# Kernel tuning notes

Measured on AMD Instinct MI355X. Metric: run time of the kernel, lower is better.

Reference implementation:

```python
import jax, jax.numpy as jnp
import numpy as np

B, L, D, C = 1, 512, 128, 128  # batch, length, input_dim, channel_dim


def _layernorm(x, w, b, eps=1e-5):
    mu = jnp.mean(x, axis=-1, keepdims=True)
    var = jnp.var(x, axis=-1, keepdims=True)
    return (x - mu) * jax.lax.rsqrt(var + eps) * w + b


def setup_inputs() -> dict:
    key = jax.random.key(0)
    ks = jax.random.split(key, 12)
    s = 0.05  # weight scale ~ xavier for d=128
    f32 = jnp.float32
    return {
        "z": jax.random.normal(ks[0], (B, L, L, D), f32),
        "ln_in_w": jnp.ones((D,), f32), "ln_in_b": jnp.zeros((D,), f32),
        "Wga": jax.random.normal(ks[1], (D, C), f32) * s, "bga": jnp.zeros((C,), f32),
        "Wla": jax.random.normal(ks[2], (D, C), f32) * s, "bla": jnp.zeros((C,), f32),
        "Wgb": jax.random.normal(ks[3], (D, C), f32) * s, "bgb": jnp.zeros((C,), f32),
        "Wlb": jax.random.normal(ks[4], (D, C), f32) * s, "blb": jnp.zeros((C,), f32),
        "ln_o_w": jnp.ones((C,), f32), "ln_o_b": jnp.zeros((C,), f32),
        "Wgo": jax.random.normal(ks[5], (D, D), f32) * s, "bgo": jnp.zeros((D,), f32),
        "Wlo": jax.random.normal(ks[6], (C, D), f32) * s, "blo": jnp.zeros((D,), f32),
    }


def reference(z, ln_in_w, ln_in_b, Wga, bga, Wla, bla, Wgb, bgb, Wlb, blb,
              ln_o_w, ln_o_b, Wgo, bgo, Wlo, blo):
    # z: [B, L, L, D]
    zn = _layernorm(z, ln_in_w, ln_in_b)
    a = jax.nn.sigmoid(zn @ Wga + bga) * (zn @ Wla + bla)   # [B,L,L,C]
    b = jax.nn.sigmoid(zn @ Wgb + bgb) * (zn @ Wlb + blb)   # [B,L,L,C]
    # triangular update (axis=1): per-channel L x L matmul
    # k[b,i,j,c] = sum_m a[b,i,m,c] * b[b,m,j,c]
    k = jnp.einsum('bimc,bmjc->bijc', a, b)
    out = jax.nn.sigmoid(zn @ Wgo + bgo) * (_layernorm(k, ln_o_w, ln_o_b) @ Wlo + blo)
    return out
```

## Files before the change

### kernel.cpp

```cpp
#include <hip/hip_runtime.h>

typedef unsigned short u16;
typedef __attribute__((ext_vector_type(8))) short bf16x8;
typedef __attribute__((ext_vector_type(4))) float f32x4;

#define L_ 512
#define D_ 128
#define LL_ (512*512)
#define LP_ 136
#define TP_ 72

#define WT_OFF 0
#define B2_OFF 98304
#define ZN_OFF (B2_OFF + 1536)
#define AT2_OFF (ZN_OFF + 128*LL_)
#define BT2_OFF (AT2_OFF + 128*LL_)
#define KT2_OFF (BT2_OFF + 128*LL_)
#define WS2_NEED_BYTES ((size_t)(KT2_OFF + 128*LL_) * 2)
#define AT1_OFF (B2_OFF + 1536)
#define BT1_OFF (AT1_OFF + 128*LL_)
#define KT1_OFF (BT1_OFF + 128*LL_)

union U16x8 { uint4 u4; bf16x8 v; u16 s[8]; };
union U16x4 { ushort4 v; u16 s[4]; };

__device__ __forceinline__ u16 f2bf(float f){
  union { float f; unsigned int i; } w; w.f = f;
  unsigned int r = w.i + 0x7FFFu + ((w.i >> 16) & 1u);
  return (u16)(r >> 16);
}
__device__ __forceinline__ float sigm(float x){
  return 1.0f / (1.0f + __expf(-x));
}

__global__ __launch_bounds__(256) void conv_kernel(
    const float* __restrict__ Wga, const float* __restrict__ Wla,
    const float* __restrict__ Wgb, const float* __restrict__ Wlb,
    const float* __restrict__ Wgo, const float* __restrict__ Wlo,
    const float* __restrict__ lnw, const float* __restrict__ lnb,
    const float* __restrict__ onw, const float* __restrict__ onb,
    const float* __restrict__ bga, const float* __restrict__ bla,
    const float* __restrict__ bgb, const float* __restrict__ blb,
    const float* __restrict__ bgo, const float* __restrict__ blo,
    u16* __restrict__ wt, float* __restrict__ bias2)
{
  if (blockIdx.x < 384){
    int idx = blockIdx.x*256 + threadIdx.x;
    int w = idx >> 14, rem = idx & 16383, n = rem >> 7, k = rem & 127;
    const float* src;
    switch (w){
      case 0: src = Wga; break; case 1: src = Wla; break; case 2: src = Wgb; break;
      case 3: src = Wlb; break; case 4: src = Wgo; break; default: src = Wlo;
    }
    float sc = (w == 5) ? onw[k] : lnw[k];
    wt[idx] = f2bf(src[k*128 + n] * sc);
  } else {
    int j = (blockIdx.x - 384)*256 + threadIdx.x;
    int w = j >> 7, n = j & 127;
    const float* src; const float* bs;
    switch (w){
      case 0: src = Wga; bs = bga; break; case 1: src = Wla; bs = bla; break;
      case 2: src = Wgb; bs = bgb; break; case 3: src = Wlb; bs = blb; break;
      case 4: src = Wgo; bs = bgo; break; default: src = Wlo; bs = blo;
    }
    const float* lb = (w == 5) ? onb : lnb;
    float acc = bs[n];
    for (int k = 0; k < 128; ++k) acc += lb[k] * src[k*128 + n];
    bias2[j] = acc;
  }
}

__global__ __launch_bounds__(256) void stageZ_kernel(
    const float* __restrict__ z, u16* __restrict__ zn_g)
{
  const int t = threadIdx.x, r = t >> 1, h = t & 1;
  const int row = blockIdx.x*128 + r;
  const float* zrow = z + (long)row*D_ + h*64;
  float raw[64];
  float sum = 0.f, sq = 0.f;
#pragma unroll
  for (int q = 0; q < 16; ++q){
    float4 v = *(const float4*)(zrow + q*4);
    raw[q*4+0] = v.x; raw[q*4+1] = v.y; raw[q*4+2] = v.z; raw[q*4+3] = v.w;
    sum += v.x + v.y + v.z + v.w;
    sq  += v.x*v.x + v.y*v.y + v.z*v.z + v.w*v.w;
  }
  sum += __shfl_xor(sum, 1, 64);
  sq  += __shfl_xor(sq , 1, 64);
  float mu = sum * (1.f/128.f);
  float rstd = rsqrtf(sq*(1.f/128.f) - mu*mu + 1e-5f);
  u16* orow = zn_g + (long)row*D_ + h*64;
#pragma unroll
  for (int q = 0; q < 8; ++q){
    U16x8 o;
#pragma unroll
    for (int e = 0; e < 8; ++e)
      o.s[e] = f2bf(raw[q*8+e] - mu > 0 ? (raw[q*8+e] - mu)*rstd : (raw[q*8+e] - mu)*rstd);
    *(uint4*)(orow + q*8) = o.u4;
  }
}

__device__ __forceinline__ void gemm128(const u16* znlds, const u16* __restrict__ wtm,
                                        int wm, int wn, int quad, int l16, f32x4 acc[4][4])
{
  bf16x8 bf[4][4];
#pragma unroll
  for (int nt = 0; nt < 4; ++nt){
    int n = wn*64 + nt*16 + l16;
#pragma unroll
    for (int kc = 0; kc < 4; ++kc){
      U16x8 u; u.u4 = *(const uint4*)(wtm + n*128 + kc*32 + quad*8);
      bf[nt][kc] = u.v;
    }
  }
#pragma unroll
  for (int mt = 0; mt < 4; ++mt){
    int row = wm*64 + mt*16 + l16;
    bf16x8 af[4];
#pragma unroll
    for (int kc = 0; kc < 4; ++kc)
      af[kc] = *(const bf16x8*)(znlds + row*LP_ + kc*32 + quad*8);
#pragma unroll
    for (int nt = 0; nt < 4; ++nt)
#pragma unroll
      for (int kc = 0; kc < 4; ++kc)
        acc[mt][nt] = __builtin_amdgcn_mfma_f32_16x16x32_bf16(af[kc], bf[nt][kc], acc[mt][nt], 0, 0, 0);
  }
}

__device__ __forceinline__ void gemm128s(const u16* znS, const u16* __restrict__ wtm,
                                         int wm, int wn, int quad, int l16, f32x4 acc[4][4])
{
  bf16x8 bf[4][4];
#pragma unroll
  for (int nt = 0; nt < 4; ++nt){
    int n = wn*64 + nt*16 + l16;
#pragma unroll
    for (int kc = 0; kc < 4; ++kc){
      U16x8 u; u.u4 = *(const uint4*)(wtm + n*128 + kc*32 + quad*8);
      bf[nt][kc] = u.v;
    }
  }
  const int r7 = l16 & 7;
#pragma unroll
  for (int mt = 0; mt < 4; ++mt){
    int row = wm*64 + mt*16 + l16;
    bf16x8 af[4];
#pragma unroll
    for (int kc = 0; kc < 4; ++kc)
      af[kc] = *(const bf16x8*)(znS + row*128 + (((kc*4 + quad) ^ r7) << 3));
#pragma unroll
    for (int nt = 0; nt < 4; ++nt)
#pragma unroll
      for (int kc = 0; kc < 4; ++kc)
        acc[mt][nt] = __builtin_amdgcn_mfma_f32_16x16x32_bf16(af[kc], bf[nt][kc], acc[mt][nt], 0, 0, 0);
  }
}

__device__ __forceinline__ void gemm64(const u16* alds, const u16* __restrict__ wtm,
                                       int wm, int wn, int quad, int l16, f32x4 acc[2][4])
{
  bf16x8 bf[4][4];
#pragma unroll
  for (int nt = 0; nt < 4; ++nt){
    int n = wn*64 + nt*16 + l16;
#pragma unroll
    for (int kc = 0; kc < 4; ++kc){
      U16x8 u; u.u4 = *(const uint4*)(wtm + n*128 + kc*32 + quad*8);
      bf[nt][kc] = u.v;
    }
  }
#pragma unroll
  for (int mt = 0; mt < 2; ++mt){
    int row = wm*32 + mt*16 + l16;
    bf16x8 af[4];
#pragma unroll
    for (int kc = 0; kc < 4; ++kc)
      af[kc] = *(const bf16x8*)(alds + row*LP_ + kc*32 + quad*8);
#pragma unroll
    for (int nt = 0; nt < 4; ++nt)
#pragma unroll
      for (int kc = 0; kc < 4; ++kc)
        acc[mt][nt] = __builtin_amdgcn_mfma_f32_16x16x32_bf16(af[kc], bf[nt][kc], acc[mt][nt], 0, 0, 0);
  }
}

__global__ __launch_bounds__(256) void stageA2_kernel(
    const u16* __restrict__ zn_g, const u16* __restrict__ wt,
    const float* __restrict__ bias2,
    u16* __restrict__ a_t, u16* __restrict__ b_tt)
{
  __shared__ __align__(16) u16 znS[128*128];

  const int bid = blockIdx.x;
  const int type = bid >> 11;
  const int tile = bid & 2047;
  const int outer = tile >> 2;
  const int seg = tile & 3;

  const int t = threadIdx.x;
  const int r = t >> 1, h = t & 1;
  const int lane = t & 63, wave = t >> 6;
  const int quad = lane >> 4, l16 = lane & 15;
  const int wm = wave & 1, wn = wave >> 1;

  {
    const int lr = lane >> 4, lc = lane & 15;
    const int r7s = (wave*4 + lr) & 7;
    const int cgx = lc ^ r7s;
#pragma unroll
    for (int q = 0; q < 8; ++q){
      int row = q*16 + wave*4 + lr;
      int gpos = (type == 0) ? (outer*L_ + seg*128 + row) : ((seg*128 + row)*L_ + outer);
      __builtin_amdgcn_global_load_lds(
          (const __attribute__((address_space(1))) void*)(zn_g + (long)gpos*D_ + cgx*8),
          (__attribute__((address_space(3))) void*)(&znS[(q*16 + wave*4)*128]),
          16, 0, 0);
    }
  }
  __syncthreads();

  const u16* wg   = wt + (type ? 2 : 0)*16384;
  const u16* wl   = wt + (type ? 3 : 1)*16384;
  const float* bgp = bias2 + (type ? 2 : 0)*128;
  const float* blp = bias2 + (type ? 3 : 1)*128;
  const f32x4 z4 = {0.f, 0.f, 0.f, 0.f};

  f32x4 accG[4][4], accL[4][4];
#pragma unroll
  for (int mt = 0; mt < 4; ++mt)
#pragma unroll
    for (int nt = 0; nt < 4; ++nt){ accG[mt][nt] = z4; accL[mt][nt] = z4; }

  gemm128s(znS, wg, wm, wn, quad, l16, accG);
#pragma unroll
  for (int nt = 0; nt < 4; ++nt){
    float bb = bgp[wn*64 + nt*16 + l16];
#pragma unroll
    for (int mt = 0; mt < 4; ++mt)
#pragma unroll
      for (int e = 0; e < 4; ++e)
        accG[mt][nt][e] = sigm(accG[mt][nt][e] + bb);
  }
  gemm128s(znS, wl, wm, wn, quad, l16, accL);
#pragma unroll
  for (int nt = 0; nt < 4; ++nt){
    float bb = blp[wn*64 + nt*16 + l16];
#pragma unroll
    for (int mt = 0; mt < 4; ++mt)
#pragma unroll
      for (int e = 0; e < 4; ++e)
        accG[mt][nt][e] *= (accL[mt][nt][e] + bb);
  }

  __syncthreads();

  u16* trh = znS;
  u16* dst = type ? b_tt : a_t;
  const int base = outer*L_ + seg*128;
#pragma unroll
  for (int pass = 0; pass < 2; ++pass){
    if (wm == pass){
#pragma unroll
      for (int nt = 0; nt < 4; ++nt){
        int gcol = wn*64 + nt*16 + l16;
#pragma unroll
        for (int mt = 0; mt < 4; ++mt){
          U16x4 pk;
#pragma unroll
          for (int e = 0; e < 4; ++e)
            pk.s[e] = f2bf(accG[mt][nt][e]);
          *(ushort4*)(trh + gcol*TP_ + mt*16 + quad*4) = pk.v;
        }
      }
    }
    __syncthreads();
#pragma unroll
    for (int q = 0; q < 4; ++q){
      uint4 v = *(const uint4*)(trh + r*TP_ + h*32 + q*8);
      *(uint4*)(dst + r*LL_ + base + pass*64 + h*32 + q*8) = v;
    }
    __syncthreads();
  }
}

__global__ __launch_bounds__(256) void stageA_kernel(
    const float* __restrict__ z, const u16* __restrict__ wt,
    const float* __restrict__ bias2,
    u16* __restrict__ a_t, u16* __restrict__ b_tt)
{
  __shared__ __align__(16) u16 smem[128*LP_];
  u16* zn = smem;
  u16* trh = smem;

  const int bid = blockIdx.x;
  const int type = bid >> 11;
  const int tile = bid & 2047;
  const int outer = tile >> 2;
  const int seg = tile & 3;

  const int t = threadIdx.x;
  const int r = t >> 1, h = t & 1;
  const int lane = t & 63, wave = t >> 6;
  const int quad = lane >> 4, l16 = lane & 15;
  const int wm = wave & 1, wn = wave >> 1;

  {
    int gpos = (type == 0) ? (outer*L_ + seg*128 + r) : ((seg*128 + r)*L_ + outer);
    const float* zrow = z + gpos*D_ + h*64;
    float raw[64];
    float sum = 0.f, sq = 0.f;
#pragma unroll
    for (int q = 0; q < 16; ++q){
      float4 v = *(const float4*)(zrow + q*4);
      raw[q*4+0] = v.x; raw[q*4+1] = v.y; raw[q*4+2] = v.z; raw[q*4+3] = v.w;
      sum += v.x + v.y + v.z + v.w;
      sq  += v.x*v.x + v.y*v.y + v.z*v.z + v.w*v.w;
    }
    sum += __shfl_xor(sum, 1, 64);
    sq  += __shfl_xor(sq , 1, 64);
    float mu = sum * (1.f/128.f);
    float rstd = rsqrtf(sq*(1.f/128.f) - mu*mu + 1e-5f);
#pragma unroll
    for (int q = 0; q < 8; ++q){
      U16x8 o;
#pragma unroll
      for (int e = 0; e < 8; ++e)
        o.s[e] = f2bf((raw[q*8+e] - mu)*rstd);
      *(uint4*)(zn + r*LP_ + h*64 + q*8) = o.u4;
    }
  }
  __syncthreads();

  const u16* wg   = wt + (type ? 2 : 0)*16384;
  const u16* wl   = wt + (type ? 3 : 1)*16384;
  const float* bgp = bias2 + (type ? 2 : 0)*128;
  const float* blp = bias2 + (type ? 3 : 1)*128;
  const f32x4 z4 = {0.f, 0.f, 0.f, 0.f};

  f32x4 accG[4][4], accL[4][4];
#pragma unroll
  for (int mt = 0; mt < 4; ++mt)
#pragma unroll
    for (int nt = 0; nt < 4; ++nt){ accG[mt][nt] = z4; accL[mt][nt] = z4; }

  gemm128(zn, wg, wm, wn, quad, l16, accG);
#pragma unroll
  for (int nt = 0; nt < 4; ++nt){
    float bb = bgp[wn*64 + nt*16 + l16];
#pragma unroll
    for (int mt = 0; mt < 4; ++mt)
#pragma unroll
      for (int e = 0; e < 4; ++e)
        accG[mt][nt][e] = sigm(accG[mt][nt][e] + bb);
  }
  gemm128(zn, wl, wm, wn, quad, l16, accL);
#pragma unroll
  for (int nt = 0; nt < 4; ++nt){
    float bb = blp[wn*64 + nt*16 + l16];
#pragma unroll
    for (int mt = 0; mt < 4; ++mt)
#pragma unroll
      for (int e = 0; e < 4; ++e)
        accG[mt][nt][e] *= (accL[mt][nt][e] + bb);
  }

  __syncthreads();

  u16* dst = type ? b_tt : a_t;
  const int base = outer*L_ + seg*128;
#pragma unroll
  for (int pass = 0; pass < 2; ++pass){
    if (wm == pass){
#pragma unroll
      for (int nt = 0; nt < 4; ++nt){
        int gcol = wn*64 + nt*16 + l16;
#pragma unroll
        for (int mt = 0; mt < 4; ++mt){
          U16x4 pk;
#pragma unroll
          for (int e = 0; e < 4; ++e)
            pk.s[e] = f2bf(accG[mt][nt][e]);
          *(ushort4*)(trh + gcol*TP_ + mt*16 + quad*4) = pk.v;
        }
      }
    }
    __syncthreads();
#pragma unroll
    for (int q = 0; q < 4; ++q){
      uint4 v = *(const uint4*)(trh + r*TP_ + h*32 + q*8);
      *(uint4*)(dst + r*LL_ + base + pass*64 + h*32 + q*8) = v;
    }
    __syncthreads();
  }
}

__global__ __launch_bounds__(256) void stageT_kernel(
    const u16* __restrict__ a_t, const u16* __restrict__ b_tt, u16* __restrict__ k_t)
{
  __shared__ __align__(16) u16 As[128*64];
  __shared__ __align__(16) u16 Bs[128*64];
  const int bid = blockIdx.x;
  const int lid = (bid & 7)*256 + (bid >> 3);
  const int c = lid >> 4, it = (lid >> 2) & 3, jt = lid & 3;
  const u16* Ab = a_t + c*LL_ + it*128*L_;
  const u16* Bb = b_tt + c*LL_ + jt*128*L_;
  const int t = threadIdx.x;
  const int lane = t & 63, wave = t >> 6;
  const int quad = lane >> 4, l16 = lane & 15;
  const int wm = wave & 1, wn = wave >> 1;
  const int sr8 = lane >> 3, scl = lane & 7;
  const int cgx = scl ^ sr8;
  const int swz = (l16 & 7) << 3;

  f32x4 acc[4][4];
  const f32x4 z4 = {0.f,0.f,0.f,0.f};
#pragma unroll
  for (int mt = 0; mt < 4; ++mt)
#pragma unroll
    for (int nt = 0; nt < 4; ++nt) acc[mt][nt] = z4;

  for (int kt = 0; kt < 8; ++kt){
    const int k0 = kt*64;
#pragma unroll
    for (int q = 0; q < 4; ++q){
      int row = q*32 + wave*8 + sr8;
      __builtin_amdgcn_global_load_lds(
          (const __attribute__((address_space(1))) void*)(Ab + row*L_ + k0 + cgx*8),
          (__attribute__((address_space(3))) void*)(&As[(q*32 + wave*8)*64]),
          16, 0, 0);
    }
#pragma unroll
    for (int q = 0; q < 4; ++q){
      int row = q*32 + wave*8 + sr8;
      __builtin_amdgcn_global_load_lds(
          (const __attribute__((address_space(1))) void*)(Bb + row*L_ + k0 + cgx*8),
          (__attribute__((address_space(3))) void*)(&Bs[(q*32 + wave*8)*64]),
          16, 0, 0);
    }
    __syncthreads();
    bf16x8 bfr[4][2];
#pragma unroll
    for (int nt = 0; nt < 4; ++nt){
      int brow = wn*64 + nt*16 + l16;
#pragma unroll
      for (int ks = 0; ks < 2; ++ks)
        bfr[nt][ks] = *(const bf16x8*)(Bs + brow*64 + (((ks*4 + quad)*8) ^ swz));
    }
#pragma unroll
    for (int mt = 0; mt < 4; ++mt){
      int arow = wm*64 + mt*16 + l16;
      bf16x8 af[2];
#pragma unroll
      for (int ks = 0; ks < 2; ++ks)
        af[ks] = *(const bf16x8*)(As + arow*64 + (((ks*4 + quad)*8) ^ swz));
#pragma unroll
      for (int nt = 0; nt < 4; ++nt)
#pragma unroll
        for (int ks = 0; ks < 2; ++ks)
          acc[mt][nt] = __builtin_amdgcn_mfma_f32_16x16x32_bf16(af[ks], bfr[nt][ks], acc[mt][nt], 0, 0, 0);
    }
    __syncthreads();
  }

#pragma unroll
  for (int mt = 0; mt < 4; ++mt)
#pragma unroll
    for (int nt = 0; nt < 4; ++nt){
      int gcol = wn*64 + nt*16 + l16;
#pragma unroll
      for (int e = 0; e < 4; ++e){
        int grow = wm*64 + mt*16 + quad*4 + e;
        k_t[c*LL_ + (it*128 + grow)*L_ + jt*128 + gcol] = f2bf(acc[mt][nt][e]);
      }
    }
}

__global__ __launch_bounds__(256) void stageC2_kernel(
    const u16* __restrict__ k_t, const u16* __restrict__ zn_g,
    const u16* __restrict__ wt, const float* __restrict__ bias2,
    float* __restrict__ out)
{
  __shared__ __align__(16) u16 zn2[64*LP_];
  __shared__ __align__(16) u16 kbuf[128*TP_];
  const u16* wtgo = wt + 4*16384;
  const u16* wtlo = wt + 5*16384;
  const float* bgo2 = bias2 + 4*128;
  const float* blo2 = bias2 + 5*128;
  const int bx = blockIdx.x;
  const int pos0 = (bx >> 3)*L_ + (bx & 7)*64;
  const int t = threadIdx.x, r = t >> 1, h = t & 1;
  const int rl4 = t >> 2, qd = t & 3;
  const int lane = t & 63, wave = t >> 6;
  const int quad = lane >> 4, l16 = lane & 15;
  const int wm = wave & 1, wn = wave >> 1;

#pragma unroll
  for (int q = 0; q < 4; ++q)
    *(uint4*)(kbuf + r*TP_ + h*32 + q*8) = *(const uint4*)(k_t + r*LL_ + pos0 + h*32 + q*8);
  __syncthreads();

  {
    float sum = 0.f, sq = 0.f;
    float kv[32];
#pragma unroll
    for (int q = 0; q < 32; ++q){
      union { unsigned int i; float f; } w;
      w.i = ((unsigned int)kbuf[(qd*32 + q)*TP_ + rl4]) << 16;
      kv[q] = w.f; sum += w.f; sq += w.f*w.f;
    }
    sum += __shfl_xor(sum, 1, 64); sq += __shfl_xor(sq, 1, 64);
    sum += __shfl_xor(sum, 2, 64); sq += __shfl_xor(sq, 2, 64);
    float mu = sum*(1.f/128.f);
    float rstd = rsqrtf(sq*(1.f/128.f) - mu*mu + 1e-5f);
#pragma unroll
    for (int q = 0; q < 4; ++q){
      U16x8 o;
#pragma unroll
      for (int e = 0; e < 8; ++e)
        o.s[e] = f2bf((kv[q*8+e] - mu)*rstd);
      *(uint4*)(zn2 + rl4*LP_ + qd*32 + q*8) = o.u4;
    }
  }
  __syncthreads();

  {
    const u16* zr = zn_g + (long)(pos0 + rl4)*D_ + qd*32;
    *(uint4*)(kbuf + rl4*LP_ + qd*32     ) = *(const uint4*)(zr);
    *(uint4*)(kbuf + rl4*LP_ + qd*32 + 8 ) = *(const uint4*)(zr + 8);
    *(uint4*)(kbuf + rl4*LP_ + qd*32 + 16) = *(const uint4*)(zr + 16);
    *(uint4*)(kbuf + rl4*LP_ + qd*32 + 24) = *(const uint4*)(zr + 24);
  }
  __syncthreads();

  f32x4 accK[2][4], accO[2][4];
  const f32x4 z4 = {0.f,0.f,0.f,0.f};
#pragma unroll
  for (int mt = 0; mt < 2; ++mt)
#pragma unroll
    for (int nt = 0; nt < 4; ++nt){ accK[mt][nt] = z4; accO[mt][nt] = z4; }

  gemm64(zn2,  wtlo, wm, wn, quad, l16, accK);
  gemm64(kbuf, wtgo, wm, wn, quad, l16, accO);

#pragma unroll
  for (int nt = 0; nt < 4; ++nt){
    int gcol = wn*64 + nt*16 + l16;
    float bo = bgo2[gcol], bl = blo2[gcol];
#pragma unroll
    for (int mt = 0; mt < 2; ++mt)
#pragma unroll
      for (int e = 0; e < 4; ++e){
        int grow = wm*32 + mt*16 + quad*4 + e;
        float s = sigm(accO[mt][nt][e] + bo);
        out[(pos0 + grow)*D_ + gcol] = s*(accK[mt][nt][e] + bl);
      }
  }
}

__global__ __launch_bounds__(256) void stageC_kernel(
    const u16* __restrict__ k_t, const float* __restrict__ z,
    const u16* __restrict__ wt, const float* __restrict__ bias2,
    float* __restrict__ out)
{
  __shared__ __align__(16) u16 zn2[64*LP_];
  __shared__ __align__(16) u16 kbuf[128*TP_];
  const u16* wtgo = wt + 4*16384;
  const u16* wtlo = wt + 5*16384;
  const float* bgo2 = bias2 + 4*128;
  const float* blo2 = bias2 + 5*128;
  const int bx = blockIdx.x;
  const int pos0 = (bx >> 3)*L_ + (bx & 7)*64;
  const int t = threadIdx.x, r = t >> 1, h = t & 1;
  const int rl4 = t >> 2, qd = t & 3;
  const int lane = t & 63, wave = t >> 6;
  const int quad = lane >> 4, l16 = lane & 15;
  const int wm = wave & 1, wn = wave >> 1;

#pragma unroll
  for (int q = 0; q < 4; ++q)
    *(uint4*)(kbuf + r*TP_ + h*32 + q*8) = *(const uint4*)(k_t + r*LL_ + pos0 + h*32 + q*8);
  __syncthreads();

  {
    float sum = 0.f, sq = 0.f;
    float kv[32];
#pragma unroll
    for (int q = 0; q < 32; ++q){
      union { unsigned int i; float f; } w;
      w.i = ((unsigned int)kbuf[(qd*32 + q)*TP_ + rl4]) << 16;
      kv[q] = w.f; sum += w.f; sq += w.f*w.f;
    }
    sum += __shfl_xor(sum, 1, 64); sq += __shfl_xor(sq, 1, 64);
    sum += __shfl_xor(sum, 2, 64); sq += __shfl_xor(sq, 2, 64);
    float mu = sum*(1.f/128.f);
    float rstd = rsqrtf(sq*(1.f/128.f) - mu*mu + 1e-5f);
#pragma unroll
    for (int q = 0; q < 4; ++q){
      U16x8 o;
#pragma unroll
      for (int e = 0; e < 8; ++e)
        o.s[e] = f2bf((kv[q*8+e] - mu)*rstd);
      *(uint4*)(zn2 + rl4*LP_ + qd*32 + q*8) = o.u4;
    }
  }
  __syncthreads();

  {
    const float* zr = z + (pos0 + rl4)*D_ + qd*32;
    float zv[32];
    float sum = 0.f, sq = 0.f;
#pragma unroll
    for (int q = 0; q < 8; ++q){
      float4 v = *(const float4*)(zr + q*4);
      zv[q*4+0] = v.x; zv[q*4+1] = v.y; zv[q*4+2] = v.z; zv[q*4+3] = v.w;
      sum += v.x + v.y + v.z + v.w;
      sq  += v.x*v.x + v.y*v.y + v.z*v.z + v.w*v.w;
    }
    sum += __shfl_xor(sum, 1, 64); sq += __shfl_xor(sq, 1, 64);
    sum += __shfl_xor(sum, 2, 64); sq += __shfl_xor(sq, 2, 64);
    float mu = sum*(1.f/128.f);
    float rstd = rsqrtf(sq*(1.f/128.f) - mu*mu + 1e-5f);
#pragma unroll
    for (int q = 0; q < 4; ++q){
      U16x8 o;
#pragma unroll
      for (int e = 0; e < 8; ++e)
        o.s[e] = f2bf((zv[q*8+e] - mu)*rstd);
      *(uint4*)(kbuf + rl4*LP_ + qd*32 + q*8) = o.u4;
    }
  }
  __syncthreads();

  f32x4 accK[2][4], accO[2][4];
  const f32x4 z4 = {0.f,0.f,0.f,0.f};
#pragma unroll
  for (int mt = 0; mt < 2; ++mt)
#pragma unroll
    for (int nt = 0; nt < 4; ++nt){ accK[mt][nt] = z4; accO[mt][nt] = z4; }

  gemm64(zn2,  wtlo, wm, wn, quad, l16, accK);
  gemm64(kbuf, wtgo, wm, wn, quad, l16, accO);

#pragma unroll
  for (int nt = 0; nt < 4; ++nt){
    int gcol = wn*64 + nt*16 + l16;
    float bo = bgo2[gcol], bl = blo2[gcol];
#pragma unroll
    for (int mt = 0; mt < 2; ++mt)
#pragma unroll
      for (int e = 0; e < 4; ++e){
        int grow = wm*32 + mt*16 + quad*4 + e;
        float s = sigm(accO[mt][nt][e] + bo);
        out[(pos0 + grow)*D_ + gcol] = s*(accK[mt][nt][e] + bl);
      }
  }
}

extern "C" void kernel_launch(void* const* d_in, const int* in_sizes, int n_in,
                              void* d_out, int out_size, void* d_ws, size_t ws_size,
                              hipStream_t stream)
{
  const float* z   = (const float*)d_in[0];
  const float* lnw = (const float*)d_in[1];
  const float* lnb = (const float*)d_in[2];
  const float* Wga = (const float*)d_in[3];
  const float* bga = (const float*)d_in[4];
  const float* Wla = (const float*)d_in[5];
  const float* bla = (const float*)d_in[6];
  const float* Wgb = (const float*)d_in[7];
  const float* bgb = (const float*)d_in[8];
  const float* Wlb = (const float*)d_in[9];
  const float* blb = (const float*)d_in[10];
  const float* onw = (const float*)d_in[11];
  const float* onb = (const float*)d_in[12];
  const float* Wgo = (const float*)d_in[13];
  const float* bgo = (const float*)d_in[14];
  const float* Wlo = (const float*)d_in[15];
  const float* blo = (const float*)d_in[16];

  u16* ws   = (u16*)d_ws;
  u16* wt   = ws + WT_OFF;
  float* b2 = (float*)(ws + B2_OFF);
  float* out = (float*)d_out;

  conv_kernel<<<387, 256, 0, stream>>>(Wga, Wla, Wgb, Wlb, Wgo, Wlo,
                                       lnw, lnb, onw, onb,
                                       bga, bla, bgb, blb, bgo, blo, wt, b2);

  if (ws_size >= WS2_NEED_BYTES){
    u16* zn_g = ws + ZN_OFF;
    u16* a_t  = ws + AT2_OFF;
    u16* b_tt = ws + BT2_OFF;
    u16* k_t  = ws + KT2_OFF;
    stageZ_kernel<<<2048, 256, 0, stream>>>(z, zn_g);
    stageA2_kernel<<<4096, 256, 0, stream>>>(zn_g, wt, b2, a_t, b_tt);
    stageT_kernel<<<2048, 256, 0, stream>>>(a_t, b_tt, k_t);
    stageC2_kernel<<<4096, 256, 0, stream>>>(k_t, zn_g, wt, b2, out);
  } else {
    u16* a_t  = ws + AT1_OFF;
    u16* b_tt = ws + BT1_OFF;
    u16* k_t  = ws + KT1_OFF;
    stageA_kernel<<<4096, 256, 0, stream>>>(z, wt, b2, a_t, b_tt);
    stageT_kernel<<<2048, 256, 0, stream>>>(a_t, b_tt, k_t);
    stageC_kernel<<<4096, 256, 0, stream>>>(k_t, z, wt, b2, out);
  }
}
```

Baseline: 576.2 us.

## Merge weight conversion into layernorm kernel, restructure stage A2 and C2 GEMM loops

```diff
diff --git a/kernel.cpp b/kernel.cpp
--- a/kernel.cpp
+++ b/kernel.cpp
@@ -33,6 +33,75 @@
   return 1.0f / (1.0f + __expf(-x));
 }
 
+__global__ __launch_bounds__(256) void convZ_kernel(
+    const float* __restrict__ z, u16* __restrict__ zn_g,
+    const float* __restrict__ Wga, const float* __restrict__ Wla,
+    const float* __restrict__ Wgb, const float* __restrict__ Wlb,
+    const float* __restrict__ Wgo, const float* __restrict__ Wlo,
+    const float* __restrict__ lnw, const float* __restrict__ lnb,
+    const float* __restrict__ onw, const float* __restrict__ onb,
+    const float* __restrict__ bga, const float* __restrict__ bla,
+    const float* __restrict__ bgb, const float* __restrict__ blb,
+    const float* __restrict__ bgo, const float* __restrict__ blo,
+    u16* __restrict__ wt, float* __restrict__ bias2)
+{
+  if (blockIdx.x < 2048){
+    const int t = threadIdx.x, r = t >> 1, h = t & 1;
+    const int row = blockIdx.x*128 + r;
+    const float* zrow = z + (long)row*D_ + h*64;
+    float raw[64];
+    float sum = 0.f, sq = 0.f;
+#pragma unroll
+    for (int q = 0; q < 16; ++q){
+      float4 v = *(const float4*)(zrow + q*4);
+      raw[q*4+0] = v.x; raw[q*4+1] = v.y; raw[q*4+2] = v.z; raw[q*4+3] = v.w;
+      sum += v.x + v.y + v.z + v.w;
+      sq  += v.x*v.x + v.y*v.y + v.z*v.z + v.w*v.w;
+    }
+    sum += __shfl_xor(sum, 1, 64);
+    sq  += __shfl_xor(sq , 1, 64);
+    float mu = sum * (1.f/128.f);
+    float rstd = rsqrtf(sq*(1.f/128.f) - mu*mu + 1e-5f);
+    u16* orow = zn_g + (long)row*D_ + h*64;
+#pragma unroll
+    for (int q = 0; q < 8; ++q){
+      U16x8 o;
+#pragma unroll
+      for (int e = 0; e < 8; ++e)
+        o.s[e] = f2bf((raw[q*8+e] - mu)*rstd);
+      *(uint4*)(orow + q*8) = o.u4;
+    }
+    return;
+  }
+  int vb = blockIdx.x - 2048;
+  if (vb < 384){
+    int idx = vb*256 + threadIdx.x;
+    int w = idx >> 14, rem = idx & 16383, n = rem >> 7, k = rem & 127;
+    const float* src;
+    switch (w){
+      case 0: src = Wga; break; case 1: src = Wla; break; case 2: src = Wgb; break;
+      case 3: src = Wlb; break; case 4: src = Wgo; break; default: src = Wlo;
+    }
+    float sc = (w == 5) ? onw[k] : lnw[k];
+    wt[idx] = f2bf(src[k*128 + n] * sc);
+  } else {
+    int j = (vb - 384)*256 + threadIdx.x;
+    if (j < 768){
+      int w = j >> 7, n = j & 127;
+      const float* src; const float* bs;
+      switch (w){
+        case 0: src = Wga; bs = bga; break; case 1: src = Wla; bs = bla; break;
+        case 2: src = Wgb; bs = bgb; break; case 3: src = Wlb; bs = blb; break;
+        case 4: src = Wgo; bs = bgo; break; default: src = Wlo; bs = blo;
+      }
+      const float* lb = (w == 5) ? onb : lnb;
+      float acc = bs[n];
+      for (int k = 0; k < 128; ++k) acc += lb[k] * src[k*128 + n];
+      bias2[j] = acc;
+    }
+  }
+}
+
 __global__ __launch_bounds__(256) void conv_kernel(
     const float* __restrict__ Wga, const float* __restrict__ Wla,
     const float* __restrict__ Wgb, const float* __restrict__ Wlb,
@@ -70,36 +139,6 @@
   }
 }
 
-__global__ __launch_bounds__(256) void stageZ_kernel(
-    const float* __restrict__ z, u16* __restrict__ zn_g)
-{
-  const int t = threadIdx.x, r = t >> 1, h = t & 1;
-  const int row = blockIdx.x*128 + r;
-  const float* zrow = z + (long)row*D_ + h*64;
-  float raw[64];
-  float sum = 0.f, sq = 0.f;
-#pragma unroll
-  for (int q = 0; q < 16; ++q){
-    float4 v = *(const float4*)(zrow + q*4);
-    raw[q*4+0] = v.x; raw[q*4+1] = v.y; raw[q*4+2] = v.z; raw[q*4+3] = v.w;
-    sum += v.x + v.y + v.z + v.w;
-    sq  += v.x*v.x + v.y*v.y + v.z*v.z + v.w*v.w;
-  }
-  sum += __shfl_xor(sum, 1, 64);
-  sq  += __shfl_xor(sq , 1, 64);
-  float mu = sum * (1.f/128.f);
-  float rstd = rsqrtf(sq*(1.f/128.f) - mu*mu + 1e-5f);
-  u16* orow = zn_g + (long)row*D_ + h*64;
-#pragma unroll
-  for (int q = 0; q < 8; ++q){
-    U16x8 o;
-#pragma unroll
-    for (int e = 0; e < 8; ++e)
-      o.s[e] = f2bf(raw[q*8+e] - mu > 0 ? (raw[q*8+e] - mu)*rstd : (raw[q*8+e] - mu)*rstd);
-    *(uint4*)(orow + q*8) = o.u4;
-  }
-}
-
 __device__ __forceinline__ void gemm128(const u16* znlds, const u16* __restrict__ wtm,
                                         int wm, int wn, int quad, int l16, f32x4 acc[4][4])
 {
@@ -120,35 +159,6 @@
 #pragma unroll
     for (int kc = 0; kc < 4; ++kc)
       af[kc] = *(const bf16x8*)(znlds + row*LP_ + kc*32 + quad*8);
-#pragma unroll
-    for (int nt = 0; nt < 4; ++nt)
-#pragma unroll
-      for (int kc = 0; kc < 4; ++kc)
-        acc[mt][nt] = __builtin_amdgcn_mfma_f32_16x16x32_bf16(af[kc], bf[nt][kc], acc[mt][nt], 0, 0, 0);
-  }
-}
-
-__device__ __forceinline__ void gemm128s(const u16* znS, const u16* __restrict__ wtm,
-                                         int wm, int wn, int quad, int l16, f32x4 acc[4][4])
-{
-  bf16x8 bf[4][4];
-#pragma unroll
-  for (int nt = 0; nt < 4; ++nt){
-    int n = wn*64 + nt*16 + l16;
-#pragma unroll
-    for (int kc = 0; kc < 4; ++kc){
-      U16x8 u; u.u4 = *(const uint4*)(wtm + n*128 + kc*32 + quad*8);
-      bf[nt][kc] = u.v;
-    }
-  }
-  const int r7 = l16 & 7;
-#pragma unroll
-  for (int mt = 0; mt < 4; ++mt){
-    int row = wm*64 + mt*16 + l16;
-    bf16x8 af[4];
-#pragma unroll
-    for (int kc = 0; kc < 4; ++kc)
-      af[kc] = *(const bf16x8*)(znS + row*128 + (((kc*4 + quad) ^ r7) << 3));
 #pragma unroll
     for (int nt = 0; nt < 4; ++nt)
 #pragma unroll
@@ -224,33 +234,44 @@
   const u16* wl   = wt + (type ? 3 : 1)*16384;
   const float* bgp = bias2 + (type ? 2 : 0)*128;
   const float* blp = bias2 + (type ? 3 : 1)*128;
-  const f32x4 z4 = {0.f, 0.f, 0.f, 0.f};
-
-  f32x4 accG[4][4], accL[4][4];
-#pragma unroll
-  for (int mt = 0; mt < 4; ++mt)
-#pragma unroll
-    for (int nt = 0; nt < 4; ++nt){ accG[mt][nt] = z4; accL[mt][nt] = z4; }
-
-  gemm128s(znS, wg, wm, wn, quad, l16, accG);
+  const int r7 = l16 & 7;
+
+  unsigned int pk[4][4][2];
 #pragma unroll
   for (int nt = 0; nt < 4; ++nt){
-    float bb = bgp[wn*64 + nt*16 + l16];
-#pragma unroll
-    for (int mt = 0; mt < 4; ++mt)
-#pragma unroll
-      for (int e = 0; e < 4; ++e)
-        accG[mt][nt][e] = sigm(accG[mt][nt][e] + bb);
-  }
-  gemm128s(znS, wl, wm, wn, quad, l16, accL);
-#pragma unroll
-  for (int nt = 0; nt < 4; ++nt){
-    float bb = blp[wn*64 + nt*16 + l16];
-#pragma unroll
-    for (int mt = 0; mt < 4; ++mt)
-#pragma unroll
-      for (int e = 0; e < 4; ++e)
-        accG[mt][nt][e] *= (accL[mt][nt][e] + bb);
+    const int n = wn*64 + nt*16 + l16;
+    bf16x8 bg[4], blw[4];
+#pragma unroll
+    for (int kc = 0; kc < 4; ++kc){
+      U16x8 u; u.u4 = *(const uint4*)(wg + n*128 + kc*32 + quad*8); bg[kc]  = u.v;
+      U16x8 v; v.u4 = *(const uint4*)(wl + n*128 + kc*32 + quad*8); blw[kc] = v.v;
+    }
+    f32x4 aG[4], aL[4];
+#pragma unroll
+    for (int mt = 0; mt < 4; ++mt){
+      aG[mt] = (f32x4){0.f,0.f,0.f,0.f};
+      aL[mt] = (f32x4){0.f,0.f,0.f,0.f};
+    }
+#pragma unroll
+    for (int mt = 0; mt < 4; ++mt){
+      const int row = wm*64 + mt*16 + l16;
+#pragma unroll
+      for (int kc = 0; kc < 4; ++kc){
+        bf16x8 af = *(const bf16x8*)(znS + row*128 + (((kc*4 + quad) ^ r7) << 3));
+        aG[mt] = __builtin_amdgcn_mfma_f32_16x16x32_bf16(af, bg[kc],  aG[mt], 0, 0, 0);
+        aL[mt] = __builtin_amdgcn_mfma_f32_16x16x32_bf16(af, blw[kc], aL[mt], 0, 0, 0);
+      }
+    }
+    const float bbG = bgp[n], bbL = blp[n];
+#pragma unroll
+    for (int mt = 0; mt < 4; ++mt){
+      float v0 = sigm(aG[mt][0] + bbG) * (aL[mt][0] + bbL);
+      float v1 = sigm(aG[mt][1] + bbG) * (aL[mt][1] + bbL);
+      float v2 = sigm(aG[mt][2] + bbG) * (aL[mt][2] + bbL);
+      float v3 = sigm(aG[mt][3] + bbG) * (aL[mt][3] + bbL);
+      pk[nt][mt][0] = (unsigned)f2bf(v0) | ((unsigned)f2bf(v1) << 16);
+      pk[nt][mt][1] = (unsigned)f2bf(v2) | ((unsigned)f2bf(v3) << 16);
+    }
   }
 
   __syncthreads();
@@ -266,11 +287,8 @@
         int gcol = wn*64 + nt*16 + l16;
 #pragma unroll
         for (int mt = 0; mt < 4; ++mt){
-          U16x4 pk;
-#pragma unroll
-          for (int e = 0; e < 4; ++e)
-            pk.s[e] = f2bf(accG[mt][nt][e]);
-          *(ushort4*)(trh + gcol*TP_ + mt*16 + quad*4) = pk.v;
+          uint2 w2; w2.x = pk[nt][mt][0]; w2.y = pk[nt][mt][1];
+          *(uint2*)(trh + gcol*TP_ + mt*16 + quad*4) = w2;
         }
       }
     }
@@ -377,11 +395,11 @@
         int gcol = wn*64 + nt*16 + l16;
 #pragma unroll
         for (int mt = 0; mt < 4; ++mt){
-          U16x4 pk;
+          U16x4 pk4;
 #pragma unroll
           for (int e = 0; e < 4; ++e)
-            pk.s[e] = f2bf(accG[mt][nt][e]);
-          *(ushort4*)(trh + gcol*TP_ + mt*16 + quad*4) = pk.v;
+            pk4.s[e] = f2bf(accG[mt][nt][e]);
+          *(ushort4*)(trh + gcol*TP_ + mt*16 + quad*4) = pk4.v;
         }
       }
     }
@@ -481,24 +499,45 @@
     const u16* __restrict__ wt, const float* __restrict__ bias2,
     float* __restrict__ out)
 {
+  __shared__ __align__(16) u16 kl[128*64];
+  __shared__ __align__(16) u16 znp[64*128];
   __shared__ __align__(16) u16 zn2[64*LP_];
-  __shared__ __align__(16) u16 kbuf[128*TP_];
   const u16* wtgo = wt + 4*16384;
   const u16* wtlo = wt + 5*16384;
   const float* bgo2 = bias2 + 4*128;
   const float* blo2 = bias2 + 5*128;
   const int bx = blockIdx.x;
   const int pos0 = (bx >> 3)*L_ + (bx & 7)*64;
-  const int t = threadIdx.x, r = t >> 1, h = t & 1;
+  const int t = threadIdx.x;
   const int rl4 = t >> 2, qd = t & 3;
   const int lane = t & 63, wave = t >> 6;
   const int quad = lane >> 4, l16 = lane & 15;
   const int wm = wave & 1, wn = wave >> 1;
 
 #pragma unroll
-  for (int q = 0; q < 4; ++q)
-    *(uint4*)(kbuf + r*TP_ + h*32 + q*8) = *(const uint4*)(k_t + r*LL_ + pos0 + h*32 + q*8);
-  __syncthreads();
+  for (int q = 0; q < 4; ++q){
+    int base = q*256 + wave*64;
+    int idx = base + lane;
+    int c = idx >> 3, ch = idx & 7;
+    __builtin_amdgcn_global_load_lds(
+        (const __attribute__((address_space(1))) void*)(k_t + (long)c*LL_ + pos0 + ch*8),
+        (__attribute__((address_space(3))) void*)(&kl[base*8]),
+        16, 0, 0);
+  }
+#pragma unroll
+  for (int q = 0; q < 4; ++q){
+    int base = q*256 + wave*64;
+    int idx = base + lane;
+    int j = idx >> 4, ch = idx & 15;
+    int chx = ch ^ (j & 7);
+    __builtin_amdgcn_global_load_lds(
+        (const __attribute__((address_space(1))) void*)(zn_g + (long)(pos0 + j)*D_ + chx*8),
+        (__attribute__((address_space(3))) void*)(&znp[base*8]),
+        16, 0, 0);
+  }
+  asm volatile("s_waitcnt vmcnt(4)" ::: "memory");
+  __builtin_amdgcn_s_barrier();
+  asm volatile("" ::: "memory");
 
   {
     float sum = 0.f, sq = 0.f;
@@ -506,7 +545,7 @@
 #pragma unroll
     for (int q = 0; q < 32; ++q){
       union { unsigned int i; float f; } w;
-      w.i = ((unsigned int)kbuf[(qd*32 + q)*TP_ + rl4]) << 16;
+      w.i = ((unsigned int)kl[(qd*32 + q)*64 + rl4]) << 16;
       kv[q] = w.f; sum += w.f; sq += w.f*w.f;
     }
     sum += __shfl_xor(sum, 1, 64); sq += __shfl_xor(sq, 1, 64);
@@ -524,36 +563,41 @@
   }
   __syncthreads();
 
-  {
-    const u16* zr = zn_g + (long)(pos0 + rl4)*D_ + qd*32;
-    *(uint4*)(kbuf + rl4*LP_ + qd*32     ) = *(const uint4*)(zr);
-    *(uint4*)(kbuf + rl4*LP_ + qd*32 + 8 ) = *(const uint4*)(zr + 8);
-    *(uint4*)(kbuf + rl4*LP_ + qd*32 + 16) = *(const uint4*)(zr + 16);
-    *(uint4*)(kbuf + rl4*LP_ + qd*32 + 24) = *(const uint4*)(zr + 24);
-  }
-  __syncthreads();
-
-  f32x4 accK[2][4], accO[2][4];
-  const f32x4 z4 = {0.f,0.f,0.f,0.f};
-#pragma unroll
-  for (int mt = 0; mt < 2; ++mt)
-#pragma unroll
-    for (int nt = 0; nt < 4; ++nt){ accK[mt][nt] = z4; accO[mt][nt] = z4; }
-
-  gemm64(zn2,  wtlo, wm, wn, quad, l16, accK);
-  gemm64(kbuf, wtgo, wm, wn, quad, l16, accO);
-
+  const int r7 = l16 & 7;
 #pragma unroll
   for (int nt = 0; nt < 4; ++nt){
-    int gcol = wn*64 + nt*16 + l16;
-    float bo = bgo2[gcol], bl = blo2[gcol];
+    const int gcol = wn*64 + nt*16 + l16;
+    bf16x8 bk[4], bo[4];
+#pragma unroll
+    for (int kc = 0; kc < 4; ++kc){
+      U16x8 u; u.u4 = *(const uint4*)(wtlo + gcol*128 + kc*32 + quad*8); bk[kc] = u.v;
+      U16x8 v; v.u4 = *(const uint4*)(wtgo + gcol*128 + kc*32 + quad*8); bo[kc] = v.v;
+    }
+    f32x4 aK[2], aO[2];
+#pragma unroll
+    for (int mt = 0; mt < 2; ++mt){
+      aK[mt] = (f32x4){0.f,0.f,0.f,0.f};
+      aO[mt] = (f32x4){0.f,0.f,0.f,0.f};
+    }
+#pragma unroll
+    for (int mt = 0; mt < 2; ++mt){
+      const int row = wm*32 + mt*16 + l16;
+#pragma unroll
+      for (int kc = 0; kc < 4; ++kc){
+        bf16x8 afK = *(const bf16x8*)(zn2 + row*LP_ + kc*32 + quad*8);
+        aK[mt] = __builtin_amdgcn_mfma_f32_16x16x32_bf16(afK, bk[kc], aK[mt], 0, 0, 0);
+        bf16x8 afO = *(const bf16x8*)(znp + row*128 + (((kc*4 + quad) ^ r7) << 3));
+        aO[mt] = __builtin_amdgcn_mfma_f32_16x16x32_bf16(afO, bo[kc], aO[mt], 0, 0, 0);
+      }
+    }
+    const float bO = bgo2[gcol], bK = blo2[gcol];
 #pragma unroll
     for (int mt = 0; mt < 2; ++mt)
 #pragma unroll
       for (int e = 0; e < 4; ++e){
         int grow = wm*32 + mt*16 + quad*4 + e;
-        float s = sigm(accO[mt][nt][e] + bo);
-        out[(pos0 + grow)*D_ + gcol] = s*(accK[mt][nt][e] + bl);
+        float s = sigm(aO[mt][e] + bO);
+        out[(pos0 + grow)*D_ + gcol] = s*(aK[mt][e] + bK);
       }
   }
 }
@@ -684,16 +728,15 @@
   float* b2 = (float*)(ws + B2_OFF);
   float* out = (float*)d_out;
 
-  conv_kernel<<<387, 256, 0, stream>>>(Wga, Wla, Wgb, Wlb, Wgo, Wlo,
-                                       lnw, lnb, onw, onb,
-                                       bga, bla, bgb, blb, bgo, blo, wt, b2);
-
   if (ws_size >= WS2_NEED_BYTES){
     u16* zn_g = ws + ZN_OFF;
     u16* a_t  = ws + AT2_OFF;
     u16* b_tt = ws + BT2_OFF;
     u16* k_t  = ws + KT2_OFF;
-    stageZ_kernel<<<2048, 256, 0, stream>>>(z, zn_g);
+    convZ_kernel<<<2435, 256, 0, stream>>>(z, zn_g,
+                                           Wga, Wla, Wgb, Wlb, Wgo, Wlo,
+                                           lnw, lnb, onw, onb,
+                                           bga, bla, bgb, blb, bgo, blo, wt, b2);
     stageA2_kernel<<<4096, 256, 0, stream>>>(zn_g, wt, b2, a_t, b_tt);
     stageT_kernel<<<2048, 256, 0, stream>>>(a_t, b_tt, k_t);
     stageC2_kernel<<<4096, 256, 0, stream>>>(k_t, zn_g, wt, b2, out);
@@ -701,6 +744,9 @@
     u16* a_t  = ws + AT1_OFF;
     u16* b_tt = ws + BT1_OFF;
     u16* k_t  = ws + KT1_OFF;
+    conv_kernel<<<387, 256, 0, stream>>>(Wga, Wla, Wgb, Wlb, Wgo, Wlo,
+                                         lnw, lnb, onw, onb,
+                                         bga, bla, bgb, blb, bgo, blo, wt, b2);
     stageA_kernel<<<4096, 256, 0, stream>>>(z, wt, b2, a_t, b_tt);
     stageT_kernel<<<2048, 256, 0, stream>>>(a_t, b_tt, k_t);
     stageC_kernel<<<4096, 256, 0, stream>>>(k_t, z, wt, b2, out);
```

Result: faster. 526.1 us (-8.7%).
